# Optimization experiments

Measured on AMD Instinct MI355X. Metric: run time of the kernel, lower is better.

The kernel has to match this reference:

```python
import jax, jax.numpy as jnp
import numpy as np

B, L, M, H, VN, VK = 128, 30, 10, 256, 32000, 2000
VT = VN + VK


def setup_inputs() -> dict:
    key = jax.random.key(0)
    ks = jax.random.split(key, 24)
    p = lambda k, shape: jax.random.normal(k, shape, jnp.float32) * 0.02
    eye = jnp.eye(H, dtype=jnp.float32)
    return {
        "sentence": jax.random.randint(ks[0], (B, L, 1), 0, VN),
        "keywords": jax.random.randint(ks[1], (B, M, 1), VN, VT),
        "categories": jax.random.randint(ks[2], (B, M, 1), VN, VT),
        "memory_size": jax.random.randint(ks[3], (B,), 1, M + 1),
        "use_teacher_forcing": 1,
        "emb": p(ks[4], (VT, H)),
        "W_ct": p(ks[5], (H, 5 * H)), "b_ct": jnp.zeros((H,), jnp.float32),
        "W_ih": p(ks[6], (4 * H, H)), "W_hh": p(ks[7], (4 * H, H)),
        "b_ih": jnp.zeros((4 * H,), jnp.float32), "b_hh": jnp.zeros((4 * H,), jnp.float32),
        "W_n": eye + p(ks[8], (H, H)), "W_k": eye + p(ks[9], (H, H)), "W_v": eye + p(ks[10], (H, H)),
        "W_nv": p(ks[11], (VN, H)), "b_nv": jnp.zeros((VN,), jnp.float32),
        "W_g": p(ks[12], (1, H)), "b_g": jnp.zeros((1,), jnp.float32),
        "W_hn": p(ks[13], (L, (L + 1) * H)), "b_hn": jnp.zeros((L,), jnp.float32),
        "W_hk": p(ks[14], (L, (L + 1) * H)), "b_hk": jnp.zeros((L,), jnp.float32),
        "W_hv": p(ks[15], (L, (L + 1) * H)), "b_hv": jnp.zeros((L,), jnp.float32),
        "W_mk": p(ks[16], (M, 4 * H)), "b_mk": jnp.zeros((M,), jnp.float32),
        "W_mv": p(ks[17], (M, 4 * H)), "b_mv": jnp.zeros((M,), jnp.float32),
    }


def _forward(sentence, keywords, categories, memory_size, use_teacher_forcing,
             emb, W_ct, b_ct, W_ih, W_hh, b_ih, b_hh, W_n, W_k, W_v,
             W_nv, b_nv, W_g, b_g, W_hn, b_hn, W_hk, b_hk, W_hv, b_hv,
             W_mk, b_mk, W_mv, b_mv):
    # prepare_memory: embed keyword/category ids, zero rows past memory_size
    ke = emb[keywords[:, :, 0]]      # (B,M,H)
    ve = emb[categories[:, :, 0]]    # (B,M,H)
    mask = (jnp.arange(M)[None, :] < memory_size[:, None])[..., None].astype(emb.dtype)
    key_mem = ke * mask
    val_mem = ve * mask
    ms = memory_size.astype(emb.dtype)[:, None]
    # prepare_history: initial hidden = (avg_mk + avg_mv)/2 at t=0
    init_h = (key_mem.sum(1) + val_mem.sum(1)) / (2.0 * ms)  # (B,H)
    hist0 = jnp.zeros((B, L, H), emb.dtype).at[:, 0, :].set(init_h)

    toks = sentence[:, 1:, 0].T          # (L-1, B) teacher tokens
    dis = jnp.arange(1, L)

    def step(carry, xs):
        histN, histK, histV, prev_h, prev_emb, loss = carry
        di, tok = xs

        def attn_h(hist, W, b):
            q = jnp.concatenate([prev_h, hist.reshape(B, -1)], axis=1)  # (B,(L+1)H)
            w = jnp.tanh(q @ W.T + b)                                    # (B,L)
            return jnp.einsum('bl,blh->bh', w, hist)

        cHN = attn_h(histN, W_hn, b_hn)
        cHK = attn_h(histK, W_hk, b_hk)
        cHV = attn_h(histV, W_hv, b_hv)
        cH = jnp.concatenate([cHN, cHK, cHV], axis=1)  # (B,3H)
        q_m = jnp.concatenate([prev_h, cH], axis=1)    # (B,4H)

        def attn_m(mem, W, b):
            w = jnp.tanh(q_m @ W.T + b)                # (B,M)
            return jnp.einsum('bm,bmh->bh', w, mem)

        cMK = attn_m(key_mem, W_mk, b_mk)
        cMV = attn_m(val_mem, W_mv, b_mv)
        # W_Ct_reshape(cat 5H) -> LSTM initial cell state
        c0 = jnp.concatenate([cH, cMK, cMV], axis=1) @ W_ct.T + b_ct  # (B,H)
        # single-step LSTM (torch gate order i,f,g,o)
        gates = prev_emb @ W_ih.T + b_ih + prev_h @ W_hh.T + b_hh
        gi, gf, gg, go = jnp.split(gates, 4, axis=1)
        c = jax.nn.sigmoid(gf) * c0 + jax.nn.sigmoid(gi) * jnp.tanh(gg)
        h = jax.nn.sigmoid(go) * jnp.tanh(c)           # (B,H)

        hN = h @ W_n.T
        hK = h @ W_k.T
        hV = h @ W_v.T
        histN = histN.at[:, di, :].set(hN)
        histK = histK.at[:, di, :].set(hK)
        histV = histV.at[:, di, :].set(hV)

        P_N = jax.nn.softmax(hN @ W_nv.T + b_nv, axis=1)                       # (B,VN)
        P_MK = jax.nn.softmax(jnp.einsum('bmh,bh->bm', key_mem, hK), axis=1)   # (B,M)
        P_MV = jax.nn.softmax(jnp.einsum('bmh,bh->bm', val_mem, hV), axis=1)
        P_M = 0.5 * (P_MK + P_MV)
        gt = jax.nn.sigmoid(h @ W_g.T + b_g)           # (B,1)
        P = jnp.concatenate([P_N * gt, P_M * (1.0 - gt)], axis=1)
        p_tok = jnp.take_along_axis(P, tok[:, None], axis=1)[:, 0]
        loss = loss - jnp.log(p_tok).sum()
        prev_emb = emb[tok]                            # teacher forcing
        return (histN, histK, histV, h, prev_emb, loss), gt

    carry0 = (hist0, hist0, hist0, init_h, emb[sentence[:, 0, 0]],
              jnp.zeros((), emb.dtype))
    carry, gs = jax.lax.scan(step, carry0, (dis, toks))
    loss = carry[5]
    g_history = jnp.zeros((B, L, 1), emb.dtype).at[:, 1:, :].set(
        jnp.transpose(gs, (1, 0, 2)))
    return loss, g_history


def reference(sentence, keywords, categories, memory_size, use_teacher_forcing,
              emb, W_ct, b_ct, W_ih, W_hh, b_ih, b_hh, W_n, W_k, W_v,
              W_nv, b_nv, W_g, b_g, W_hn, b_hn, W_hk, b_hk, W_hv, b_hv,
              W_mk, b_mk, W_mv, b_mv):
    return _forward(sentence, keywords, categories, memory_size, use_teacher_forcing,
                    emb, W_ct, b_ct, W_ih, W_hh, b_ih, b_hh, W_n, W_k, W_v,
                    W_nv, b_nv, W_g, b_g, W_hn, b_hn, W_hk, b_hk, W_hv, b_hv,
                    W_mk, b_mk, W_mv, b_mv)
```

## Files before the change

### kernel.cpp

```cpp
#include <hip/hip_runtime.h>
#include <math.h>

#define B_ 128
#define L_ 30
#define M_ 10
#define H_ 256
#define VN_ 32000
#define NCHK 500
#define NG 3712

typedef __bf16 bf16;
typedef bf16 bf16x8 __attribute__((ext_vector_type(8)));
typedef float f32x4 __attribute__((ext_vector_type(4)));

#define MFMA(a,b,c) __builtin_amdgcn_mfma_f32_16x16x32_bf16(a, b, c, 0, 0, 0)

__device__ __forceinline__ float rcpf(float x) { return __builtin_amdgcn_rcpf(x); }
__device__ __forceinline__ float sigf(float x) { return rcpf(1.f + __expf(-x)); }
__device__ __forceinline__ float ftanh(float x) {
  float e = __expf(2.f * x);
  return 1.f - 2.f * rcpf(e + 1.f);
}
__device__ __forceinline__ float u2lo(unsigned w) { return __builtin_bit_cast(float, w << 16); }
__device__ __forceinline__ float u2hi(unsigned w) { return __builtin_bit_cast(float, w & 0xffff0000u); }
__device__ __forceinline__ unsigned packbf2(float a, float b) {
  unsigned short lo = __builtin_bit_cast(unsigned short, (bf16)a);
  unsigned short hi = __builtin_bit_cast(unsigned short, (bf16)b);
  return (unsigned)lo | ((unsigned)hi << 16);
}

#if __has_builtin(__builtin_amdgcn_fdot2_f32_bf16)
typedef __bf16 bf16x2 __attribute__((ext_vector_type(2)));
__device__ __forceinline__ float dot2(unsigned x, unsigned w, float c) {
  return __builtin_amdgcn_fdot2_f32_bf16(__builtin_bit_cast(bf16x2, x),
                                         __builtin_bit_cast(bf16x2, w), c, false);
}
#else
__device__ __forceinline__ float dot2(unsigned x, unsigned w, float c) {
  c = fmaf(u2lo(x), u2lo(w), c);
  return fmaf(u2hi(x), u2hi(w), c);
}
#endif

__global__ __launch_bounds__(256) void k_prep(
    const float* W_ct, const float* W_hh,
    const float* W_n, const float* W_k, const float* W_v,
    const float* W_hn, const float* W_hk, const float* W_hv,
    const float* W_mk, const float* W_mv, const float* W_g,
    unsigned* W4g, unsigned* W4nkv, unsigned* W4ph, unsigned* WctP45,
    unsigned* W4m0, unsigned* W4qm, unsigned* W4da, unsigned* W4db, unsigned* WgP) {
  int stride = gridDim.x * blockDim.x;
  int base = blockIdx.x * blockDim.x + threadIdx.x;
  for (int idx = base; idx < 131072; idx += stride) {
    int s = idx & 3, tt = (idx >> 2) & 1023, i = idx >> 12;
    int n = 4*(tt >> 2) + s, k2 = (tt & 3) + 4*i;
    W4g[idx] = packbf2(W_hh[n*256 + 2*k2], W_hh[n*256 + 2*k2 + 1]);
  }
  for (int idx = base; idx < 98304; idx += stride) {
    int s = idx & 3, r2 = idx >> 2, tt = r2 % 768, i = r2 / 768;
    int n = 4*(tt >> 2) + s, k2 = (tt & 3) + 4*i;
    const float* src = (n < 256) ? W_n : (n < 512) ? W_k : W_v;
    int nn = n & 255;
    W4nkv[idx] = packbf2(src[nn*256 + 2*k2], src[nn*256 + 2*k2 + 1]);
  }
  for (int idx = base; idx < 98304; idx += stride) {
    int s = idx & 3, r2 = idx >> 2, q = r2 % 768, i = r2 / 768;
    int X = q >> 8, rr = q & 255, ob = rr >> 2, kq = rr & 3;
    int nl = 4*ob + s, k2 = kq + 4*i;
    int col = X*256 + 2*k2;
    W4ph[idx] = packbf2(W_ct[nl*1280 + col], W_ct[nl*1280 + col + 1]);
  }
  for (int i = base; i < 65536; i += stride) {
    int X = i >> 15, r = i & 32767, k2 = r >> 8, n = r & 255;
    int col = 768 + X*256 + 2*k2;
    WctP45[i] = packbf2(W_ct[n*1280 + col], W_ct[n*1280 + col + 1]);
  }
  for (int idx = base; idx < 4096; idx += stride) {
    int s = idx & 3, tt = (idx >> 2) & 31, i = idx >> 7;
    int c = 4*(tt >> 2) + s, k2 = (tt & 3) + 4*i;
    float x0 = 0.f, x1 = 0.f;
    if (c < 10)              { x0 = W_mk[c*1024 + 2*k2]; x1 = W_mk[c*1024 + 2*k2 + 1]; }
    else if (c >= 16 && c < 26) { int m = c-16; x0 = W_mv[m*1024 + 2*k2]; x1 = W_mv[m*1024 + 2*k2 + 1]; }
    W4m0[idx] = packbf2(x0, x1);
  }
  for (int idx = base; idx < 12288; idx += stride) {
    int s = idx & 3, r2 = idx >> 2, q = r2 % 96, i = r2 / 96;
    int X = q >> 5, r = q & 31;
    int c = 4*(r >> 2) + s, k2 = (r & 3) + 4*i;
    int off = 256 + X*256 + 2*k2;
    float x0 = 0.f, x1 = 0.f;
    if (c < 10)              { x0 = W_mk[c*1024 + off]; x1 = W_mk[c*1024 + off + 1]; }
    else if (c >= 16 && c < 26) { int m = c-16; x0 = W_mv[m*1024 + off]; x1 = W_mv[m*1024 + off + 1]; }
    W4qm[idx] = packbf2(x0, x1);
  }
  for (int idx = base; idx < 491520; idx += stride) {
    int s = idx & 3, tt = (idx >> 2) & 127, i = (idx >> 9) & 31, d = idx >> 14;
    int c = 4*(tt >> 2) + s, k2 = (tt & 3) + 4*i;
    float x0 = 0.f, x1 = 0.f;
    if (c < 96) {
      int X = c >> 5, l = c & 31;
      if (l < 30) {
        const float* W = (X == 0) ? W_hn : (X == 1) ? W_hk : W_hv;
        x0 = W[l*7936 + d*256 + 2*k2]; x1 = W[l*7936 + d*256 + 2*k2 + 1];
      }
    }
    W4da[idx] = packbf2(x0, x1);
  }
  for (int idx = base; idx < 16384; idx += stride) {
    int s = idx & 3, tt = (idx >> 2) & 127, i = idx >> 9;
    int c = 4*(tt >> 2) + s, k2 = (tt & 3) + 4*i;
    float x0 = 0.f, x1 = 0.f;
    if (c < 96) {
      int X = c >> 5, l = c & 31;
      if (l < 30) {
        const float* W = (X == 0) ? W_hn : (X == 1) ? W_hk : W_hv;
        x0 = W[l*7936 + 2*k2]; x1 = W[l*7936 + 2*k2 + 1];
      }
    }
    W4db[idx] = packbf2(x0, x1);
  }
  for (int i = base; i < 128; i += stride) WgP[i] = packbf2(W_g[2*i], W_g[2*i+1]);
}

__global__ __launch_bounds__(256) void k_pregates(
    const int* sentence, const float* emb, const float* W_ih,
    const float* b_ih, const float* b_hh, float* prehg) {
  extern __shared__ char smp[];
  char* Al = smp;
  char* Bl = smp + 65536;
  __shared__ int tok_s[128];
  int blk = blockIdx.x;
  int gd = blk >> 3, nc = blk & 7;
  int t = threadIdx.x, wid = t >> 6, lane = t & 63;
  if (t < 128) tok_s[t] = sentence[t*L_ + gd];
  __syncthreads();
  for (int i = t; i < 128*32; i += 256) {
    int r = i >> 5, c8 = i & 31;
    const float* e = emb + (size_t)tok_s[r]*H_ + c8*8;
    float4 f0 = *(const float4*)e, f1 = *(const float4*)(e + 4);
    int4 v;
    v.x = (int)packbf2(f0.x, f0.y); v.y = (int)packbf2(f0.z, f0.w);
    v.z = (int)packbf2(f1.x, f1.y); v.w = (int)packbf2(f1.z, f1.w);
    *(int4*)(Al + ((r*512 + c8*16) ^ ((r&7)<<4))) = v;
    const float* wsrc = W_ih + (size_t)(nc*128 + r)*H_ + c8*8;
    float4 g0 = *(const float4*)wsrc, g1 = *(const float4*)(wsrc + 4);
    int4 w;
    w.x = (int)packbf2(g0.x, g0.y); w.y = (int)packbf2(g0.z, g0.w);
    w.z = (int)packbf2(g1.x, g1.y); w.w = (int)packbf2(g1.z, g1.w);
    *(int4*)(Bl + ((r*512 + c8*16) ^ ((r&7)<<4))) = w;
  }
  __syncthreads();
  f32x4 acc[2][8] = {};
  #pragma unroll 2
  for (int kk = 0; kk < 8; ++kk) {
    int kb2 = kk*64 + (lane>>4)*16;
    bf16x8 af[2], bfr[8];
    #pragma unroll
    for (int fi = 0; fi < 2; ++fi) {
      int m = wid*32 + fi*16 + (lane & 15);
      af[fi] = *(const bf16x8*)(Al + ((m*512 + kb2) ^ ((m&7)<<4)));
    }
    #pragma unroll
    for (int fj = 0; fj < 8; ++fj) {
      int n = fj*16 + (lane & 15);
      bfr[fj] = *(const bf16x8*)(Bl + ((n*512 + kb2) ^ ((n&7)<<4)));
    }
    #pragma unroll
    for (int fi = 0; fi < 2; ++fi)
      #pragma unroll
      for (int fj = 0; fj < 8; ++fj)
        acc[fi][fj] = MFMA(af[fi], bfr[fj], acc[fi][fj]);
  }
  #pragma unroll
  for (int fi = 0; fi < 2; ++fi)
    #pragma unroll
    for (int fj = 0; fj < 8; ++fj)
      #pragma unroll
      for (int r = 0; r < 4; ++r) {
        int row = wid*32 + fi*16 + (lane>>4)*4 + r;
        int col = nc*128 + fj*16 + (lane & 15);
        prehg[((size_t)gd*128 + row)*1024 + col] = acc[fi][fj][r] + b_ih[col] + b_hh[col];
      }
}

struct LoopP {
  const int *sentence, *keywords, *categories, *memsz;
  const float *emb;
  const unsigned *W4g, *W4nkv, *W4ph, *WctP45, *W4m0, *W4qm, *W4da, *W4db, *WgP;
  const float *prehg;
  const float *b_ct, *b_hn, *b_hk, *b_hv, *b_mk, *b_mv, *b_g;
  unsigned* hNb;
  unsigned* hNbT;
  float* gt_all;
  float* outg;
};

__global__ __launch_bounds__(1024) void k_loop(LoopP p) {
  extern __shared__ unsigned Su[];
  float* Sf = (float*)Su;
  const int t = threadIdx.x, b = blockIdx.x;
  enum { PH = 0, QM = 11520, P45 = 14400, MB = 16960,
         GA = 19520, HP = 20544, HV = 20672,
         SW = 21056, ACA = 21152, SWM = 21248, M0 = 21280,
         DA = 21312, DB = 21440,
         BCT = 21568, BH = 21824, BM = 21920, BG = 21952 };

  for (int i = t; i < 2560; i += 1024) {
    int X = i / 1280, r = i - X*1280, m = r >> 7, j = r & 127;
    int ms = p.memsz[b];
    int idx = (X == 0 ? p.keywords : p.categories)[b*M_ + m];
    unsigned u = 0;
    if (m < ms) {
      const float* e = p.emb + (size_t)idx*H_ + 2*j;
      u = packbf2(e[0], e[1]);
    }
    Su[MB + i] = u;
  }
  if (t < 256) Sf[BCT + t] = p.b_ct[t];
  if (t < 96) {
    int X = t >> 5, l = t & 31;
    const float* bh = (X == 0) ? p.b_hn : (X == 1) ? p.b_hk : p.b_hv;
    Sf[BH + t] = (l < 30) ? bh[l] : 0.f;
    Sf[ACA + t] = 0.f;
  }
  if (t < 32) {
    float v = 0.f;
    if (t < 10) v = p.b_mk[t];
    else if (t >= 16 && t < 26) v = p.b_mv[t - 16];
    Sf[BM + t] = v;
  }
  if (t == 0) { Sf[BG] = p.b_g[0]; p.outg[b*L_] = 0.f; }
  __syncthreads();
  if (t < 128) {
    float a0 = 0.f, a1 = 0.f;
    #pragma unroll
    for (int q = 0; q < 20; ++q) {
      unsigned u = Su[MB + q*128 + t];
      a0 += u2lo(u); a1 += u2hi(u);
    }
    float msf = (float)p.memsz[b];
    unsigned up = packbf2(a0 / (2.f * msf), a1 / (2.f * msf));
    Su[HP + t] = up;
    Su[HV + t] = up; Su[HV + 128 + t] = up; Su[HV + 256 + t] = up;
  }
  for (int q = t; q < 2560; q += 1024) {
    int X = q / 1280, r = q - X*1280, m = r >> 7, j = r & 127;
    float a0 = 0.f, a1 = 0.f;
    const uint2* wp = (const uint2*)(p.WctP45 + (X << 15)) + j;
    const unsigned* mb = Su + MB + X*1280 + m*128;
    #pragma unroll 4
    for (int k2 = 0; k2 < 128; ++k2) {
      uint2 w = wp[k2 << 7];
      unsigned u = mb[k2];
      a0 = dot2(u, w.x, a0);
      a1 = dot2(u, w.y, a1);
    }
    Su[P45 + q] = packbf2(a0, a1);
  }
  __syncthreads();

  for (int di = 1; di < L_; ++di) {
    {
      const float pre = p.prehg[(size_t)(((di-1) << 7) | b)*1024 + t];
      int kq = t & 3;
      const uint4* wr = (const uint4*)p.W4g + t;
      const unsigned* xp = Su + HP + kq;
      float p0 = 0.f, p1 = 0.f, p2 = 0.f, p3 = 0.f;
      #pragma unroll 8
      for (int i = 0; i < 32; ++i) {
        uint4 w = wr[(size_t)i << 10];
        unsigned x = xp[4*i];
        p0 = dot2(x, w.x, p0); p1 = dot2(x, w.y, p1);
        p2 = dot2(x, w.z, p2); p3 = dot2(x, w.w, p3);
      }
      p0 += __shfl_xor(p0, 1); p1 += __shfl_xor(p1, 1); p2 += __shfl_xor(p2, 1); p3 += __shfl_xor(p3, 1);
      p0 += __shfl_xor(p0, 2); p1 += __shfl_xor(p1, 2); p2 += __shfl_xor(p2, 2); p3 += __shfl_xor(p3, 2);
      float sel = (kq == 0) ? p0 : (kq == 1) ? p1 : (kq == 2) ? p2 : p3;
      Sf[GA + t] = pre + sel;
    }
    if (t < 128) {
      int kq = t & 3;
      const uint4* wr = (const uint4*)p.W4da + (size_t)di*4096 + t;
      const unsigned* xp = Su + HV + ((t >> 5) << 7) + kq;
      float p0 = 0.f, p1 = 0.f, p2 = 0.f, p3 = 0.f;
      #pragma unroll 8
      for (int i = 0; i < 32; ++i) {
        uint4 w = wr[i << 7];
        unsigned x = xp[4*i];
        p0 = dot2(x, w.x, p0); p1 = dot2(x, w.y, p1);
        p2 = dot2(x, w.z, p2); p3 = dot2(x, w.w, p3);
      }
      p0 += __shfl_xor(p0, 1); p1 += __shfl_xor(p1, 1); p2 += __shfl_xor(p2, 1); p3 += __shfl_xor(p3, 1);
      p0 += __shfl_xor(p0, 2); p1 += __shfl_xor(p1, 2); p2 += __shfl_xor(p2, 2); p3 += __shfl_xor(p3, 2);
      float sel = (kq == 0) ? p0 : (kq == 1) ? p1 : (kq == 2) ? p2 : p3;
      Sf[DA + t] = sel;
    } else if (t < 256) {
      int c = t - 128, kq = c & 3;
      const uint4* wr = (const uint4*)p.W4db + c;
      const unsigned* xp = Su + HP + kq;
      float p0 = 0.f, p1 = 0.f, p2 = 0.f, p3 = 0.f;
      #pragma unroll 8
      for (int i = 0; i < 32; ++i) {
        uint4 w = wr[i << 7];
        unsigned x = xp[4*i];
        p0 = dot2(x, w.x, p0); p1 = dot2(x, w.y, p1);
        p2 = dot2(x, w.z, p2); p3 = dot2(x, w.w, p3);
      }
      p0 += __shfl_xor(p0, 1); p1 += __shfl_xor(p1, 1); p2 += __shfl_xor(p2, 1); p3 += __shfl_xor(p3, 1);
      p0 += __shfl_xor(p0, 2); p1 += __shfl_xor(p1, 2); p2 += __shfl_xor(p2, 2); p3 += __shfl_xor(p3, 2);
      float sel = (kq == 0) ? p0 : (kq == 1) ? p1 : (kq == 2) ? p2 : p3;
      Sf[DB + c] = sel;
    } else {
      int q = t - 256;
      int X = q >> 8, rr = q & 255, ob = rr >> 2, kq = rr & 3;
      const uint4* wr = (const uint4*)p.W4ph + q;
      const unsigned* xp = Su + HV + (X << 7) + kq;
      float p0 = 0.f, p1 = 0.f, p2 = 0.f, p3 = 0.f;
      #pragma unroll 8
      for (int i = 0; i < 32; ++i) {
        uint4 w = wr[i*768];
        unsigned x = xp[4*i];
        p0 = dot2(x, w.x, p0); p1 = dot2(x, w.y, p1);
        p2 = dot2(x, w.z, p2); p3 = dot2(x, w.w, p3);
      }
      p0 += __shfl_xor(p0, 1); p1 += __shfl_xor(p1, 1); p2 += __shfl_xor(p2, 1); p3 += __shfl_xor(p3, 1);
      p0 += __shfl_xor(p0, 2); p1 += __shfl_xor(p1, 2); p2 += __shfl_xor(p2, 2); p3 += __shfl_xor(p3, 2);
      int phbase = PH + (X*30 + di-1)*128;
      if (kq == 0)       Su[phbase + 2*ob]     = packbf2(p0, p1);
      else if (kq == 2)  Su[phbase + 2*ob + 1] = packbf2(p2, p3);
    }
    __syncthreads();
    if (t < 96) {
      float a = Sf[ACA + t] + Sf[DA + t];
      Sf[ACA + t] = a;
      Sf[SW + t] = ftanh(a + Sf[DB + t] + Sf[BH + t]);
    } else if (t >= 128 && t < 224) {
      int q = t - 128, X = q >> 5, r = q & 31, kq = r & 3;
      const uint4* wr = (const uint4*)p.W4qm + q;
      const unsigned* xp = Su + HV + (X << 7) + kq;
      float p0 = 0.f, p1 = 0.f, p2 = 0.f, p3 = 0.f;
      #pragma unroll 8
      for (int i = 0; i < 32; ++i) {
        uint4 w = wr[i*96];
        unsigned x = xp[4*i];
        p0 = dot2(x, w.x, p0); p1 = dot2(x, w.y, p1);
        p2 = dot2(x, w.z, p2); p3 = dot2(x, w.w, p3);
      }
      p0 += __shfl_xor(p0, 1); p1 += __shfl_xor(p1, 1); p2 += __shfl_xor(p2, 1); p3 += __shfl_xor(p3, 1);
      p0 += __shfl_xor(p0, 2); p1 += __shfl_xor(p1, 2); p2 += __shfl_xor(p2, 2); p3 += __shfl_xor(p3, 2);
      float sel = (kq == 0) ? p0 : (kq == 1) ? p1 : (kq == 2) ? p2 : p3;
      Sf[QM + (X*30 + di-1)*32 + r] = sel;
    } else if (t >= 224 && t < 256) {
      int r = t - 224, kq = r & 3;
      const uint4* wr = (const uint4*)p.W4m0 + r;
      const unsigned* xp = Su + HP + kq;
      float p0 = 0.f, p1 = 0.f, p2 = 0.f, p3 = 0.f;
      #pragma unroll 8
      for (int i = 0; i < 32; ++i) {
        uint4 w = wr[i << 5];
        unsigned x = xp[4*i];
        p0 = dot2(x, w.x, p0); p1 = dot2(x, w.y, p1);
        p2 = dot2(x, w.z, p2); p3 = dot2(x, w.w, p3);
      }
      p0 += __shfl_xor(p0, 1); p1 += __shfl_xor(p1, 1); p2 += __shfl_xor(p2, 1); p3 += __shfl_xor(p3, 1);
      p0 += __shfl_xor(p0, 2); p1 += __shfl_xor(p1, 2); p2 += __shfl_xor(p2, 2); p3 += __shfl_xor(p3, 2);
      float sel = (kq == 0) ? p0 : (kq == 1) ? p1 : (kq == 2) ? p2 : p3;
      Sf[M0 + r] = sel;
    }
    __syncthreads();
    if (t < 32) {
      bool valid = (t < 10) || (t >= 16 && t < 26);
      if (valid) {
        float aN = 0.f, aK = 0.f, aV = 0.f;
        const float* sw0 = Sf + SW;
        const float* q0 = Sf + QM + t;
        for (int l = 0; l < di; ++l) {
          aN = fmaf(sw0[l],      q0[l*32],        aN);
          aK = fmaf(sw0[32 + l], q0[960 + l*32],  aK);
          aV = fmaf(sw0[64 + l], q0[1920 + l*32], aV);
        }
        Sf[SWM + t] = ftanh(Sf[M0 + t] + Sf[BM + t] + aN + aK + aV);
      }
    }
    __syncthreads();
    if (t < 128) {
      float a0 = Sf[BCT + 2*t], a1 = Sf[BCT + 2*t + 1];
      for (int X = 0; X < 3; ++X) {
        const float* swp = Sf + SW + X*32;
        const unsigned* php = Su + PH + X*3840 + t;
        float e0 = 0.f, e1 = 0.f, o0 = 0.f, o1 = 0.f;
        int l = 0;
        for (; l + 1 < di; l += 2) {
          float s0 = swp[l], s1 = swp[l+1];
          unsigned ua = php[l*128], ub = php[(l+1)*128];
          e0 = fmaf(s0, u2lo(ua), e0); e1 = fmaf(s0, u2hi(ua), e1);
          o0 = fmaf(s1, u2lo(ub), o0); o1 = fmaf(s1, u2hi(ub), o1);
        }
        if (l < di) {
          float s = swp[l]; unsigned u = php[l*128];
          e0 = fmaf(s, u2lo(u), e0); e1 = fmaf(s, u2hi(u), e1);
        }
        a0 += e0 + o0; a1 += e1 + o1;
      }
      {
        float pp0 = 0.f, pp1 = 0.f, qq0 = 0.f, qq1 = 0.f;
        #pragma unroll
        for (int m = 0; m < 10; ++m) {
          float sk = Sf[SWM + m], sv = Sf[SWM + 16 + m];
          unsigned uk = Su[P45 + m*128 + t], uv = Su[P45 + 1280 + m*128 + t];
          pp0 = fmaf(sk, u2lo(uk), pp0); pp1 = fmaf(sk, u2hi(uk), pp1);
          qq0 = fmaf(sv, u2lo(uv), qq0); qq1 = fmaf(sv, u2hi(uv), qq1);
        }
        a0 += pp0 + qq0; a1 += pp1 + qq1;
      }
      int n0 = 2*t;
      float gi0 = Sf[GA+n0],   gf0 = Sf[GA+256+n0], gg0 = Sf[GA+512+n0], go0 = Sf[GA+768+n0];
      float gi1 = Sf[GA+n0+1], gf1 = Sf[GA+257+n0], gg1 = Sf[GA+513+n0], go1 = Sf[GA+769+n0];
      float cc0 = sigf(gf0)*a0 + sigf(gi0)*ftanh(gg0);
      float cc1 = sigf(gf1)*a1 + sigf(gi1)*ftanh(gg1);
      float h0 = sigf(go0)*ftanh(cc0);
      float h1 = sigf(go1)*ftanh(cc1);
      Su[HP + t] = packbf2(h0, h1);
    }
    __syncthreads();
    if (t < 768) {
      int ob = t >> 2, kq = t & 3;
      const uint4* wr = (const uint4*)p.W4nkv + t;
      const unsigned* xp = Su + HP + kq;
      float p0 = 0.f, p1 = 0.f, p2 = 0.f, p3 = 0.f;
      #pragma unroll 8
      for (int i = 0; i < 32; ++i) {
        uint4 w = wr[i*768];
        unsigned x = xp[4*i];
        p0 = dot2(x, w.x, p0); p1 = dot2(x, w.y, p1);
        p2 = dot2(x, w.z, p2); p3 = dot2(x, w.w, p3);
      }
      p0 += __shfl_xor(p0, 1); p1 += __shfl_xor(p1, 1); p2 += __shfl_xor(p2, 1); p3 += __shfl_xor(p3, 1);
      p0 += __shfl_xor(p0, 2); p1 += __shfl_xor(p1, 2); p2 += __shfl_xor(p2, 2); p3 += __shfl_xor(p3, 2);
      if ((kq & 1) == 0) {
        int thv = 2*ob + (kq >> 1);
        unsigned up = (kq == 0) ? packbf2(p0, p1) : packbf2(p2, p3);
        Su[HV + thv] = up;
        if (thv < 128) {
          int tile = di - 1;
          p.hNb[(size_t)((tile << 7) | b)*128 + thv] = up;
          int idx = ((((tile*4 + (b>>5))*8 + (thv>>4))*64 + ((thv>>2)&3)*16 + (b&15))*2 + ((b>>4)&1))*4 + (thv&3);
          p.hNbT[idx] = up;
        }
      }
    } else if (t >= 768 && t < 832) {
      int j = t - 768;
      float a = dot2(Su[HP + 2*j], p.WgP[2*j], 0.f);
      a = dot2(Su[HP + 2*j + 1], p.WgP[2*j + 1], a);
      #pragma unroll
      for (int o = 1; o < 64; o <<= 1) a += __shfl_xor(a, o);
      if (j == 0) {
        float g = sigf(a + Sf[BG]);
        p.gt_all[((di-1) << 7) | b] = g;
        p.outg[b*L_ + di] = g;
      }
    }
    __syncthreads();
  }
}

__global__ __launch_bounds__(256) void k_vocab(
    const unsigned* hNbT, const float* W_nv, const float* b_nv, float2* pmps) {
  extern __shared__ char smv[];
  int ch = blockIdx.x;
  int t = threadIdx.x, wid = t >> 6, lane = t & 63;
  int v0 = ch * 64;
  for (int i = t; i < 64*32; i += 256) {
    int r = i >> 5, c8 = i & 31;
    const float* wsrc = W_nv + (size_t)(v0 + r)*H_ + c8*8;
    float4 f0 = *(const float4*)wsrc, f1 = *(const float4*)(wsrc + 4);
    int4 v;
    v.x = (int)packbf2(f0.x, f0.y); v.y = (int)packbf2(f0.z, f0.w);
    v.z = (int)packbf2(f1.x, f1.y); v.w = (int)packbf2(f1.z, f1.w);
    *(int4*)(smv + ((r*512 + c8*16) ^ ((r&7)<<4))) = v;
  }
  float bb4[4];
  #pragma unroll
  for (int fj = 0; fj < 4; ++fj) bb4[fj] = b_nv[v0 + fj*16 + (lane & 15)];
  __syncthreads();
  bf16x8 Breg[8][4];
  #pragma unroll
  for (int kk = 0; kk < 8; ++kk) {
    int kb2 = kk*64 + (lane>>4)*16;
    #pragma unroll
    for (int fj = 0; fj < 4; ++fj) {
      int n = fj*16 + (lane & 15);
      Breg[kk][fj] = *(const bf16x8*)(smv + ((n*512 + kb2) ^ ((n&7)<<4)));
    }
  }
  const int4* At = (const int4*)hNbT;
  for (int tile = 0; tile < 29; ++tile) {
    f32x4 acc[2][4] = {};
    #pragma unroll
    for (int kk = 0; kk < 8; ++kk) {
      bf16x8 af[2];
      #pragma unroll
      for (int fi = 0; fi < 2; ++fi) {
        int4 u = At[((tile*4 + wid)*8 + kk)*128 + lane*2 + fi];
        af[fi] = __builtin_bit_cast(bf16x8, u);
      }
      #pragma unroll
      for (int fi = 0; fi < 2; ++fi)
        #pragma unroll
        for (int fj = 0; fj < 4; ++fj)
          acc[fi][fj] = MFMA(af[fi], Breg[kk][fj], acc[fi][fj]);
    }
    #pragma unroll
    for (int fi = 0; fi < 2; ++fi)
      #pragma unroll
      for (int r = 0; r < 4; ++r) {
        float mi = acc[fi][0][r] + bb4[0];
        #pragma unroll
        for (int fj = 1; fj < 4; ++fj) mi = fmaxf(mi, acc[fi][fj][r] + bb4[fj]);
        for (int o = 1; o < 16; o <<= 1) mi = fmaxf(mi, __shfl_xor(mi, o));
        float si = 0.f;
        #pragma unroll
        for (int fj = 0; fj < 4; ++fj) si += __expf(acc[fi][fj][r] + bb4[fj] - mi);
        for (int o = 1; o < 16; o <<= 1) si += __shfl_xor(si, o);
        if ((lane & 15) == 0) {
          int row = wid*32 + fi*16 + (lane>>4)*4 + r;
          pmps[(size_t)(tile*128 + row)*512 + ch] = make_float2(mi, si);
        }
      }
  }
}

__global__ __launch_bounds__(128) void k_combine(
    const float2* pmps, const unsigned* hNb, const float* W_nv, const float* b_nv,
    const float* gt_all, const int* sentence, float* loss_part) {
  __shared__ float red[128];
  int tile = blockIdx.x, bb = threadIdx.x;
  int g = tile*128 + bb;
  float M = -1e30f, Ssum = 0.f;
  const float2* pv = pmps + (size_t)g*512;
  #pragma unroll 4
  for (int c = 0; c < NCHK; ++c) {
    float2 v = pv[c];
    float M2 = fmaxf(M, v.x);
    Ssum = Ssum*__expf(M - M2) + v.y*__expf(v.x - M2);
    M = M2;
  }
  int tok = sentence[bb*L_ + tile + 1];
  float z = b_nv[tok];
  const unsigned* hu = hNb + (size_t)g*128;
  const float* wr = W_nv + (size_t)tok*H_;
  #pragma unroll 8
  for (int k = 0; k < 128; ++k) {
    unsigned w2 = hu[k];
    z += u2lo(w2)*wr[2*k] + u2hi(w2)*wr[2*k + 1];
  }
  float term = -(z - M - __logf(Ssum) + __logf(gt_all[g]));
  red[bb] = term;
  __syncthreads();
  for (int o = 64; o > 0; o >>= 1) {
    if (bb < o) red[bb] += red[bb + o];
    __syncthreads();
  }
  if (bb == 0) loss_part[tile] = red[0];
}

__global__ __launch_bounds__(64) void k_fin(const float* lp, float* out) {
  int t = threadIdx.x;
  float v = (t < 29) ? lp[t] : 0.f;
  for (int o = 1; o < 64; o <<= 1) v += __shfl_xor(v, o);
  if (t == 0) out[0] = v;
}

extern "C" void kernel_launch(void* const* d_in, const int* in_sizes, int n_in,
                              void* d_out, int out_size, void* d_ws, size_t ws_size,
                              hipStream_t stream) {
  const int* sentence  = (const int*)d_in[0];
  const int* keywords  = (const int*)d_in[1];
  const int* categories= (const int*)d_in[2];
  const int* memsz     = (const int*)d_in[3];
  const float* emb  = (const float*)d_in[5];
  const float* W_ct = (const float*)d_in[6];
  const float* b_ct = (const float*)d_in[7];
  const float* W_ih = (const float*)d_in[8];
  const float* W_hh = (const float*)d_in[9];
  const float* b_ih = (const float*)d_in[10];
  const float* b_hh = (const float*)d_in[11];
  const float* W_n  = (const float*)d_in[12];
  const float* W_k  = (const float*)d_in[13];
  const float* W_v  = (const float*)d_in[14];
  const float* W_nv = (const float*)d_in[15];
  const float* b_nv = (const float*)d_in[16];
  const float* W_g  = (const float*)d_in[17];
  const float* b_g  = (const float*)d_in[18];
  const float* W_hn = (const float*)d_in[19];
  const float* b_hn = (const float*)d_in[20];
  const float* W_hk = (const float*)d_in[21];
  const float* b_hk = (const float*)d_in[22];
  const float* W_hv = (const float*)d_in[23];
  const float* b_hv = (const float*)d_in[24];
  const float* W_mk = (const float*)d_in[25];
  const float* b_mk = (const float*)d_in[26];
  const float* W_mv = (const float*)d_in[27];
  const float* b_mv = (const float*)d_in[28];
  float* out = (float*)d_out;

  char* wsp = (char*)d_ws;
  size_t off = 0;
  auto alloc = [&](size_t bytes) -> void* {
    void* pp = wsp + off;
    off = (off + bytes + 255) & ~(size_t)255;
    return pp;
  };
  unsigned* W4g    = (unsigned*)alloc((size_t)131072*4);
  unsigned* W4nkv  = (unsigned*)alloc((size_t)98304*4);
  unsigned* W4ph   = (unsigned*)alloc((size_t)98304*4);
  unsigned* WctP45 = (unsigned*)alloc((size_t)65536*4);
  unsigned* W4m0   = (unsigned*)alloc((size_t)4096*4);
  unsigned* W4qm   = (unsigned*)alloc((size_t)12288*4);
  unsigned* W4da   = (unsigned*)alloc((size_t)491520*4);
  unsigned* W4db   = (unsigned*)alloc((size_t)16384*4);
  unsigned* WgP    = (unsigned*)alloc((size_t)128*4);
  float* prehg     = (float*)alloc((size_t)29*B_*1024*4);
  unsigned* hNb    = (unsigned*)alloc((size_t)29*B_*128*4);
  unsigned* hNbT   = (unsigned*)alloc((size_t)29*B_*128*4);
  float* gt_all    = (float*)alloc((size_t)29*B_*4);
  float2* pmps     = (float2*)alloc((size_t)NG*512*8);
  float* loss_part = (float*)alloc(29*4);

  k_prep<<<512, 256, 0, stream>>>(W_ct, W_hh, W_n, W_k, W_v,
      W_hn, W_hk, W_hv, W_mk, W_mv, W_g,
      W4g, W4nkv, W4ph, WctP45, W4m0, W4qm, W4da, W4db, WgP);
  k_pregates<<<232, 256, 131072, stream>>>(sentence, emb, W_ih, b_ih, b_hh, prehg);

  LoopP P;
  P.sentence = sentence; P.keywords = keywords; P.categories = categories; P.memsz = memsz;
  P.emb = emb;
  P.W4g = W4g; P.W4nkv = W4nkv; P.W4ph = W4ph; P.WctP45 = WctP45;
  P.W4m0 = W4m0; P.W4qm = W4qm; P.W4da = W4da; P.W4db = W4db; P.WgP = WgP;
  P.prehg = prehg;
  P.b_ct = b_ct; P.b_hn = b_hn; P.b_hk = b_hk; P.b_hv = b_hv;
  P.b_mk = b_mk; P.b_mv = b_mv; P.b_g = b_g;
  P.hNb = hNb; P.hNbT = hNbT; P.gt_all = gt_all; P.outg = out + 1;

  k_loop<<<B_, 1024, 87812, stream>>>(P);
  k_vocab<<<NCHK, 256, 32768, stream>>>(hNbT, W_nv, b_nv, pmps);
  k_combine<<<29, 128, 0, stream>>>(pmps, hNb, W_nv, b_nv, gt_all, sentence, loss_part);
  k_fin<<<1, 64, 0, stream>>>(loss_part, out);
}
```

Before: 683.7 us.

## Store recurrent weights in FP8 and fuse pregates GEMM into prep kernel

```diff
diff --git a/kernel.cpp b/kernel.cpp
--- a/kernel.cpp
+++ b/kernel.cpp
@@ -12,6 +12,7 @@
 typedef __bf16 bf16;
 typedef bf16 bf16x8 __attribute__((ext_vector_type(8)));
 typedef float f32x4 __attribute__((ext_vector_type(4)));
+typedef float f32x2 __attribute__((ext_vector_type(2)));
 
 #define MFMA(a,b,c) __builtin_amdgcn_mfma_f32_16x16x32_bf16(a, b, c, 0, 0, 0)
 
@@ -42,33 +43,170 @@
 }
 #endif
 
+#if __has_builtin(__builtin_amdgcn_cvt_pk_f32_fp8) && __has_builtin(__builtin_amdgcn_cvt_pk_fp8_f32)
+template <bool HI>
+__device__ __forceinline__ f32x2 upk8(unsigned u) {
+  return __builtin_amdgcn_cvt_pk_f32_fp8((int)u, HI);
+}
+__device__ __forceinline__ unsigned pk8x4(float a, float b, float c, float d) {
+  int v = __builtin_amdgcn_cvt_pk_fp8_f32(a, b, 0, false);
+  v = __builtin_amdgcn_cvt_pk_fp8_f32(c, d, v, true);
+  return (unsigned)v;
+}
+#else
+__device__ __forceinline__ float dec8(unsigned byte) {
+  unsigned s = byte >> 7, e = (byte >> 3) & 15, m = byte & 7;
+  float v;
+  if (e == 0) v = (float)m * __builtin_bit_cast(float, (unsigned)((-9 + 127) << 23));
+  else        v = (float)(8 + m) * __builtin_bit_cast(float, (unsigned)(((int)e - 10 + 127) << 23));
+  return s ? -v : v;
+}
+template <bool HI>
+__device__ __forceinline__ f32x2 upk8(unsigned u) {
+  unsigned sh = HI ? 16u : 0u;
+  f32x2 r;
+  r.x = dec8((u >> sh) & 0xff);
+  r.y = dec8((u >> (sh + 8)) & 0xff);
+  return r;
+}
+__device__ __forceinline__ unsigned enc8(float f) {
+  if (f == 0.f || f != f) return 0;
+  unsigned b = __builtin_bit_cast(unsigned, f);
+  unsigned s = (b >> 31) << 7;
+  int e = (int)((b >> 23) & 255) - 127;
+  unsigned frac = b & 0x7fffff;
+  if (e < -6) {
+    float av = fabsf(f);
+    int m = (int)(av * 512.f + 0.5f);
+    if (m >= 8) return s | (1u << 3);
+    return s | (unsigned)m;
+  }
+  int m = (int)((frac + 0x80000u) >> 20);
+  int ee = e + 7;
+  if (m == 8) { m = 0; ee++; }
+  if (ee >= 16) { ee = 15; m = 6; }
+  return s | ((unsigned)ee << 3) | (unsigned)m;
+}
+__device__ __forceinline__ unsigned pk8x4(float a, float b, float c, float d) {
+  return enc8(a) | (enc8(b) << 8) | (enc8(c) << 16) | (enc8(d) << 24);
+}
+#endif
+
+__device__ __forceinline__ void dot8fp8(uint2 w, unsigned x,
+                                        float& p0, float& p1, float& p2, float& p3) {
+  float xl = u2lo(x), xh = u2hi(x);
+  f32x2 c0 = upk8<false>(w.x), c1 = upk8<true>(w.x);
+  f32x2 c2 = upk8<false>(w.y), c3 = upk8<true>(w.y);
+  p0 = fmaf(xl, c0.x, fmaf(xh, c0.y, p0));
+  p1 = fmaf(xl, c1.x, fmaf(xh, c1.y, p1));
+  p2 = fmaf(xl, c2.x, fmaf(xh, c2.y, p2));
+  p3 = fmaf(xl, c3.x, fmaf(xh, c3.y, p3));
+}
+
 __global__ __launch_bounds__(256) void k_prep(
     const float* W_ct, const float* W_hh,
     const float* W_n, const float* W_k, const float* W_v,
     const float* W_hn, const float* W_hk, const float* W_hv,
     const float* W_mk, const float* W_mv, const float* W_g,
-    unsigned* W4g, unsigned* W4nkv, unsigned* W4ph, unsigned* WctP45,
-    unsigned* W4m0, unsigned* W4qm, unsigned* W4da, unsigned* W4db, unsigned* WgP) {
-  int stride = gridDim.x * blockDim.x;
+    uint2* W8g, uint2* W8nkv, uint2* W8ph, unsigned* WctP45,
+    unsigned* W4m0, unsigned* W4qm, unsigned* W4da, unsigned* W4db, unsigned* WgP,
+    const int* sentence, const float* emb, const float* W_ih,
+    const float* b_ih, const float* b_hh, float* prehg) {
+  if (blockIdx.x >= 512) {
+    extern __shared__ char smp[];
+    char* Al = smp;
+    char* Bl = smp + 65536;
+    __shared__ int tok_s[128];
+    int blk = blockIdx.x - 512;
+    int gd = blk >> 3, nc = blk & 7;
+    int t = threadIdx.x, wid = t >> 6, lane = t & 63;
+    if (t < 128) tok_s[t] = sentence[t*L_ + gd];
+    __syncthreads();
+    for (int i = t; i < 128*32; i += 256) {
+      int r = i >> 5, c8 = i & 31;
+      const float* e = emb + (size_t)tok_s[r]*H_ + c8*8;
+      float4 f0 = *(const float4*)e, f1 = *(const float4*)(e + 4);
+      int4 v;
+      v.x = (int)packbf2(f0.x, f0.y); v.y = (int)packbf2(f0.z, f0.w);
+      v.z = (int)packbf2(f1.x, f1.y); v.w = (int)packbf2(f1.z, f1.w);
+      *(int4*)(Al + ((r*512 + c8*16) ^ ((r&7)<<4))) = v;
+      const float* wsrc = W_ih + (size_t)(nc*128 + r)*H_ + c8*8;
+      float4 g0 = *(const float4*)wsrc, g1 = *(const float4*)(wsrc + 4);
+      int4 w;
+      w.x = (int)packbf2(g0.x, g0.y); w.y = (int)packbf2(g0.z, g0.w);
+      w.z = (int)packbf2(g1.x, g1.y); w.w = (int)packbf2(g1.z, g1.w);
+      *(int4*)(Bl + ((r*512 + c8*16) ^ ((r&7)<<4))) = w;
+    }
+    __syncthreads();
+    f32x4 acc[2][8] = {};
+    #pragma unroll 2
+    for (int kk = 0; kk < 8; ++kk) {
+      int kb2 = kk*64 + (lane>>4)*16;
+      bf16x8 af[2], bfr[8];
+      #pragma unroll
+      for (int fi = 0; fi < 2; ++fi) {
+        int m = wid*32 + fi*16 + (lane & 15);
+        af[fi] = *(const bf16x8*)(Al + ((m*512 + kb2) ^ ((m&7)<<4)));
+      }
+      #pragma unroll
+      for (int fj = 0; fj < 8; ++fj) {
+        int n = fj*16 + (lane & 15);
+        bfr[fj] = *(const bf16x8*)(Bl + ((n*512 + kb2) ^ ((n&7)<<4)));
+      }
+      #pragma unroll
+      for (int fi = 0; fi < 2; ++fi)
+        #pragma unroll
+        for (int fj = 0; fj < 8; ++fj)
+          acc[fi][fj] = MFMA(af[fi], bfr[fj], acc[fi][fj]);
+    }
+    #pragma unroll
+    for (int fi = 0; fi < 2; ++fi)
+      #pragma unroll
+      for (int fj = 0; fj < 8; ++fj)
+        #pragma unroll
+        for (int r = 0; r < 4; ++r) {
+          int row = wid*32 + fi*16 + (lane>>4)*4 + r;
+          int col = nc*128 + fj*16 + (lane & 15);
+          prehg[((size_t)gd*128 + row)*1024 + col] = acc[fi][fj][r] + b_ih[col] + b_hh[col];
+        }
+    return;
+  }
+  int stride = 512 * blockDim.x;
   int base = blockIdx.x * blockDim.x + threadIdx.x;
-  for (int idx = base; idx < 131072; idx += stride) {
-    int s = idx & 3, tt = (idx >> 2) & 1023, i = idx >> 12;
-    int n = 4*(tt >> 2) + s, k2 = (tt & 3) + 4*i;
-    W4g[idx] = packbf2(W_hh[n*256 + 2*k2], W_hh[n*256 + 2*k2 + 1]);
-  }
-  for (int idx = base; idx < 98304; idx += stride) {
-    int s = idx & 3, r2 = idx >> 2, tt = r2 % 768, i = r2 / 768;
-    int n = 4*(tt >> 2) + s, k2 = (tt & 3) + 4*i;
-    const float* src = (n < 256) ? W_n : (n < 512) ? W_k : W_v;
-    int nn = n & 255;
-    W4nkv[idx] = packbf2(src[nn*256 + 2*k2], src[nn*256 + 2*k2 + 1]);
-  }
-  for (int idx = base; idx < 98304; idx += stride) {
-    int s = idx & 3, r2 = idx >> 2, q = r2 % 768, i = r2 / 768;
+  for (int idx = base; idx < 32768; idx += stride) {
+    int t = idx & 1023, i = idx >> 10;
+    int nb = 4*(t >> 2), k2 = (t & 3) + 4*i;
+    const float* w0 = W_hh + (size_t)nb*256 + 2*k2;
+    uint2 o;
+    o.x = pk8x4(w0[0], w0[1], w0[256], w0[257]);
+    o.y = pk8x4(w0[512], w0[513], w0[768], w0[769]);
+    W8g[idx] = o;
+  }
+  for (int idx = base; idx < 24576; idx += stride) {
+    int tt = idx % 768, i = idx / 768;
+    int nb = 4*(tt >> 2), k2 = (tt & 3) + 4*i;
+    float v[8];
+    #pragma unroll
+    for (int s = 0; s < 4; ++s) {
+      int n = nb + s;
+      const float* src = (n < 256) ? W_n : (n < 512) ? W_k : W_v;
+      int nn = n & 255;
+      v[2*s] = src[nn*256 + 2*k2]; v[2*s+1] = src[nn*256 + 2*k2 + 1];
+    }
+    uint2 o;
+    o.x = pk8x4(v[0], v[1], v[2], v[3]);
+    o.y = pk8x4(v[4], v[5], v[6], v[7]);
+    W8nkv[idx] = o;
+  }
+  for (int idx = base; idx < 24576; idx += stride) {
+    int q = idx % 768, i = idx / 768;
     int X = q >> 8, rr = q & 255, ob = rr >> 2, kq = rr & 3;
-    int nl = 4*ob + s, k2 = kq + 4*i;
-    int col = X*256 + 2*k2;
-    W4ph[idx] = packbf2(W_ct[nl*1280 + col], W_ct[nl*1280 + col + 1]);
+    int k2 = kq + 4*i, col = X*256 + 2*k2;
+    const float* w0 = W_ct + (size_t)(4*ob)*1280 + col;
+    uint2 o;
+    o.x = pk8x4(w0[0], w0[1], w0[1280], w0[1281]);
+    o.y = pk8x4(w0[2560], w0[2561], w0[3840], w0[3841]);
+    W8ph[idx] = o;
   }
   for (int i = base; i < 65536; i += stride) {
     int X = i >> 15, r = i & 32767, k2 = r >> 8, n = r & 255;
@@ -122,71 +260,11 @@
   for (int i = base; i < 128; i += stride) WgP[i] = packbf2(W_g[2*i], W_g[2*i+1]);
 }
 
-__global__ __launch_bounds__(256) void k_pregates(
-    const int* sentence, const float* emb, const float* W_ih,
-    const float* b_ih, const float* b_hh, float* prehg) {
-  extern __shared__ char smp[];
-  char* Al = smp;
-  char* Bl = smp + 65536;
-  __shared__ int tok_s[128];
-  int blk = blockIdx.x;
-  int gd = blk >> 3, nc = blk & 7;
-  int t = threadIdx.x, wid = t >> 6, lane = t & 63;
-  if (t < 128) tok_s[t] = sentence[t*L_ + gd];
-  __syncthreads();
-  for (int i = t; i < 128*32; i += 256) {
-    int r = i >> 5, c8 = i & 31;
-    const float* e = emb + (size_t)tok_s[r]*H_ + c8*8;
-    float4 f0 = *(const float4*)e, f1 = *(const float4*)(e + 4);
-    int4 v;
-    v.x = (int)packbf2(f0.x, f0.y); v.y = (int)packbf2(f0.z, f0.w);
-    v.z = (int)packbf2(f1.x, f1.y); v.w = (int)packbf2(f1.z, f1.w);
-    *(int4*)(Al + ((r*512 + c8*16) ^ ((r&7)<<4))) = v;
-    const float* wsrc = W_ih + (size_t)(nc*128 + r)*H_ + c8*8;
-    float4 g0 = *(const float4*)wsrc, g1 = *(const float4*)(wsrc + 4);
-    int4 w;
-    w.x = (int)packbf2(g0.x, g0.y); w.y = (int)packbf2(g0.z, g0.w);
-    w.z = (int)packbf2(g1.x, g1.y); w.w = (int)packbf2(g1.z, g1.w);
-    *(int4*)(Bl + ((r*512 + c8*16) ^ ((r&7)<<4))) = w;
-  }
-  __syncthreads();
-  f32x4 acc[2][8] = {};
-  #pragma unroll 2
-  for (int kk = 0; kk < 8; ++kk) {
-    int kb2 = kk*64 + (lane>>4)*16;
-    bf16x8 af[2], bfr[8];
-    #pragma unroll
-    for (int fi = 0; fi < 2; ++fi) {
-      int m = wid*32 + fi*16 + (lane & 15);
-      af[fi] = *(const bf16x8*)(Al + ((m*512 + kb2) ^ ((m&7)<<4)));
-    }
-    #pragma unroll
-    for (int fj = 0; fj < 8; ++fj) {
-      int n = fj*16 + (lane & 15);
-      bfr[fj] = *(const bf16x8*)(Bl + ((n*512 + kb2) ^ ((n&7)<<4)));
-    }
-    #pragma unroll
-    for (int fi = 0; fi < 2; ++fi)
-      #pragma unroll
-      for (int fj = 0; fj < 8; ++fj)
-        acc[fi][fj] = MFMA(af[fi], bfr[fj], acc[fi][fj]);
-  }
-  #pragma unroll
-  for (int fi = 0; fi < 2; ++fi)
-    #pragma unroll
-    for (int fj = 0; fj < 8; ++fj)
-      #pragma unroll
-      for (int r = 0; r < 4; ++r) {
-        int row = wid*32 + fi*16 + (lane>>4)*4 + r;
-        int col = nc*128 + fj*16 + (lane & 15);
-        prehg[((size_t)gd*128 + row)*1024 + col] = acc[fi][fj][r] + b_ih[col] + b_hh[col];
-      }
-}
-
 struct LoopP {
   const int *sentence, *keywords, *categories, *memsz;
   const float *emb;
-  const unsigned *W4g, *W4nkv, *W4ph, *WctP45, *W4m0, *W4qm, *W4da, *W4db, *WgP;
+  const uint2 *W8g, *W8nkv, *W8ph;
+  const unsigned *WctP45, *W4m0, *W4qm, *W4da, *W4db, *WgP;
   const float *prehg;
   const float *b_ct, *b_hn, *b_hk, *b_hv, *b_mk, *b_mv, *b_g;
   unsigned* hNb;
@@ -263,15 +341,13 @@
     {
       const float pre = p.prehg[(size_t)(((di-1) << 7) | b)*1024 + t];
       int kq = t & 3;
-      const uint4* wr = (const uint4*)p.W4g + t;
+      const uint2* wr = p.W8g + t;
       const unsigned* xp = Su + HP + kq;
       float p0 = 0.f, p1 = 0.f, p2 = 0.f, p3 = 0.f;
       #pragma unroll 8
       for (int i = 0; i < 32; ++i) {
-        uint4 w = wr[(size_t)i << 10];
-        unsigned x = xp[4*i];
-        p0 = dot2(x, w.x, p0); p1 = dot2(x, w.y, p1);
-        p2 = dot2(x, w.z, p2); p3 = dot2(x, w.w, p3);
+        uint2 w = wr[(size_t)i << 10];
+        dot8fp8(w, xp[4*i], p0, p1, p2, p3);
       }
       p0 += __shfl_xor(p0, 1); p1 += __shfl_xor(p1, 1); p2 += __shfl_xor(p2, 1); p3 += __shfl_xor(p3, 1);
       p0 += __shfl_xor(p0, 2); p1 += __shfl_xor(p1, 2); p2 += __shfl_xor(p2, 2); p3 += __shfl_xor(p3, 2);
@@ -313,15 +389,13 @@
     } else {
       int q = t - 256;
       int X = q >> 8, rr = q & 255, ob = rr >> 2, kq = rr & 3;
-      const uint4* wr = (const uint4*)p.W4ph + q;
+      const uint2* wr = p.W8ph + q;
       const unsigned* xp = Su + HV + (X << 7) + kq;
       float p0 = 0.f, p1 = 0.f, p2 = 0.f, p3 = 0.f;
       #pragma unroll 8
       for (int i = 0; i < 32; ++i) {
-        uint4 w = wr[i*768];
-        unsigned x = xp[4*i];
-        p0 = dot2(x, w.x, p0); p1 = dot2(x, w.y, p1);
-        p2 = dot2(x, w.z, p2); p3 = dot2(x, w.w, p3);
+        uint2 w = wr[i*768];
+        dot8fp8(w, xp[4*i], p0, p1, p2, p3);
       }
       p0 += __shfl_xor(p0, 1); p1 += __shfl_xor(p1, 1); p2 += __shfl_xor(p2, 1); p3 += __shfl_xor(p3, 1);
       p0 += __shfl_xor(p0, 2); p1 += __shfl_xor(p1, 2); p2 += __shfl_xor(p2, 2); p3 += __shfl_xor(p3, 2);
@@ -425,15 +499,13 @@
     __syncthreads();
     if (t < 768) {
       int ob = t >> 2, kq = t & 3;
-      const uint4* wr = (const uint4*)p.W4nkv + t;
+      const uint2* wr = p.W8nkv + t;
       const unsigned* xp = Su + HP + kq;
       float p0 = 0.f, p1 = 0.f, p2 = 0.f, p3 = 0.f;
       #pragma unroll 8
       for (int i = 0; i < 32; ++i) {
-        uint4 w = wr[i*768];
-        unsigned x = xp[4*i];
-        p0 = dot2(x, w.x, p0); p1 = dot2(x, w.y, p1);
-        p2 = dot2(x, w.z, p2); p3 = dot2(x, w.w, p3);
+        uint2 w = wr[i*768];
+        dot8fp8(w, xp[4*i], p0, p1, p2, p3);
       }
       p0 += __shfl_xor(p0, 1); p1 += __shfl_xor(p1, 1); p2 += __shfl_xor(p2, 1); p3 += __shfl_xor(p3, 1);
       p0 += __shfl_xor(p0, 2); p1 += __shfl_xor(p1, 2); p2 += __shfl_xor(p2, 2); p3 += __shfl_xor(p3, 2);
@@ -611,9 +683,9 @@
     off = (off + bytes + 255) & ~(size_t)255;
     return pp;
   };
-  unsigned* W4g    = (unsigned*)alloc((size_t)131072*4);
-  unsigned* W4nkv  = (unsigned*)alloc((size_t)98304*4);
-  unsigned* W4ph   = (unsigned*)alloc((size_t)98304*4);
+  uint2* W8g       = (uint2*)alloc((size_t)32768*8);
+  uint2* W8nkv     = (uint2*)alloc((size_t)24576*8);
+  uint2* W8ph      = (uint2*)alloc((size_t)24576*8);
   unsigned* WctP45 = (unsigned*)alloc((size_t)65536*4);
   unsigned* W4m0   = (unsigned*)alloc((size_t)4096*4);
   unsigned* W4qm   = (unsigned*)alloc((size_t)12288*4);
@@ -627,16 +699,16 @@
   float2* pmps     = (float2*)alloc((size_t)NG*512*8);
   float* loss_part = (float*)alloc(29*4);
 
-  k_prep<<<512, 256, 0, stream>>>(W_ct, W_hh, W_n, W_k, W_v,
+  k_prep<<<744, 256, 131072, stream>>>(W_ct, W_hh, W_n, W_k, W_v,
       W_hn, W_hk, W_hv, W_mk, W_mv, W_g,
-      W4g, W4nkv, W4ph, WctP45, W4m0, W4qm, W4da, W4db, WgP);
-  k_pregates<<<232, 256, 131072, stream>>>(sentence, emb, W_ih, b_ih, b_hh, prehg);
+      W8g, W8nkv, W8ph, WctP45, W4m0, W4qm, W4da, W4db, WgP,
+      sentence, emb, W_ih, b_ih, b_hh, prehg);
 
   LoopP P;
   P.sentence = sentence; P.keywords = keywords; P.categories = categories; P.memsz = memsz;
   P.emb = emb;
-  P.W4g = W4g; P.W4nkv = W4nkv; P.W4ph = W4ph; P.WctP45 = WctP45;
-  P.W4m0 = W4m0; P.W4qm = W4qm; P.W4da = W4da; P.W4db = W4db; P.WgP = WgP;
+  P.W8g = W8g; P.W8nkv = W8nkv; P.W8ph = W8ph;
+  P.WctP45 = WctP45; P.W4m0 = W4m0; P.W4qm = W4qm; P.W4da = W4da; P.W4db = W4db; P.WgP = WgP;
   P.prehg = prehg;
   P.b_ct = b_ct; P.b_hn = b_hn; P.b_hk = b_hk; P.b_hv = b_hv;
   P.b_mk = b_mk; P.b_mv = b_mv; P.b_g = b_g;
```

New measurement: 818.3 us. +19.7%, slower.
